# Kernel optimization log

Hardware: AMD Instinct MI355X
Metric: run time of the kernel (lower is better)

Reference implementation:

```python
import jax, jax.numpy as jnp
import numpy as np

D = 256        # model_dim
E = 4          # num_experts
H = 8          # attention heads
L = 8          # layers
P = 4          # patch size
IMG = 128
B = 8
NUM_CLASSES = 10
T = (IMG // P) ** 2  # 1024 tokens


def _ln(x, g, b):
    mu = jnp.mean(x, -1, keepdims=True)
    var = jnp.mean((x - mu) ** 2, -1, keepdims=True)
    return (x - mu) * jax.lax.rsqrt(var + 1e-5) * g + b


def setup_inputs() -> dict:
    key = jax.random.key(0)
    ks = jax.random.split(key, 24)
    n = lambda k, s, sc=0.02: jax.random.normal(k, s, jnp.float32) * sc
    return {
        "x": jax.random.normal(ks[0], (B, 3, IMG, IMG), jnp.float32),
        "patch_w": n(ks[1], (D, 3, P, P), 0.1),
        "patch_b": n(ks[2], (D,), 0.01),
        "pos_emb": n(ks[3], (1, T, D), 0.02),
        "router_w": n(ks[4], (E, D), 0.05),
        "router_b": n(ks[5], (E,), 0.01),
        "ln1_g": jnp.ones((L, D), jnp.float32),
        "ln1_b": jnp.zeros((L, D), jnp.float32),
        "q_w": n(ks[6], (L, D, D), 0.05),
        "q_b": n(ks[7], (L, D), 0.01),
        "k_w": n(ks[8], (L, D, D), 0.05),
        "k_b": n(ks[9], (L, D), 0.01),
        "v_w": n(ks[10], (L, D, D), 0.05),
        "v_b": n(ks[11], (L, D), 0.01),
        "o_w": n(ks[12], (L, D, D), 0.05),
        "o_b": n(ks[13], (L, D), 0.01),
        "ln2_g": jnp.ones((L, D), jnp.float32),
        "ln2_b": jnp.zeros((L, D), jnp.float32),
        "l1_w": n(ks[14], (L, 4 * D, D), 0.05),
        "l1_b": n(ks[15], (L, 4 * D), 0.01),
        "l2_w": n(ks[16], (L, D, 4 * D), 0.05),
        "l2_b": n(ks[17], (L, D), 0.01),
        "head_w": n(ks[18], (NUM_CLASSES, D), 0.05),
        "head_b": n(ks[19], (NUM_CLASSES,), 0.01),
        "alpha": jnp.full((1,), 0.5, jnp.float32),
    }


def reference(x, patch_w, patch_b, pos_emb, router_w, router_b, ln1_g, ln1_b,
              q_w, q_b, k_w, k_b, v_w, v_b, o_w, o_b, ln2_g, ln2_b,
              l1_w, l1_b, l2_w, l2_b, head_w, head_b, alpha):
    b = x.shape[0]
    # patch embed: Conv2d(3, D, P, stride=P)
    h = jax.lax.conv_general_dilated(x, patch_w, (P, P), 'VALID',
                                     dimension_numbers=('NCHW', 'OIHW', 'NCHW'))
    h = h + patch_b[None, :, None, None]
    tok = h.reshape(b, D, -1).transpose(0, 2, 1) + pos_emb   # [B,T,D]
    t = tok.shape[1]
    n_per = t // E  # uniform capacity: floor(T * 1/E)
    raw_prob = jax.nn.softmax(tok @ router_w.T + router_b, axis=-1)  # [B,T,E]
    # greedy routing: expert e takes top n_per of remaining tokens, rows zeroed after
    prob = raw_prob
    bidx = jnp.arange(b)[:, None]
    blocks, pblocks = [], []
    for e in range(E):
        _, idx = jax.lax.top_k(prob[:, :, e], n_per)            # [B,n_per]
        blocks.append(jnp.take_along_axis(tok, idx[:, :, None], axis=1))
        pblocks.append(jnp.take_along_axis(raw_prob, idx[:, :, None], axis=1))
        sel = jnp.zeros((b, t), prob.dtype).at[bidx, idx].set(1.0)
        prob = prob * (1.0 - sel)[:, :, None]
    xs = jnp.concatenate(blocks, axis=1)    # [B,T,D] expert-sorted
    rp = jnp.concatenate(pblocks, axis=1)   # [B,T,E]

    widths = [D // 2 ** e for e in range(E)]  # [256,128,64,32]
    scale = D ** -0.5                         # note: model_dim, not head_dim
    dh = D // H
    for l in range(L):
        # ---- nested-expert MHSA ----
        xn = _ln(xs, ln1_g[l], ln1_b[l])
        qs, ks_, vs = [], [], []
        for e in range(E):
            m = widths[e]
            blk = xn[:, e * n_per:(e + 1) * n_per, :m]
            qs.append(blk @ q_w[l][:, :m].T + q_b[l])
            ks_.append(blk @ k_w[l][:, :m].T + k_b[l])
            vs.append(blk @ v_w[l][:, :m].T + v_b[l])
        q = jnp.concatenate(qs, 1).reshape(b, t, H, dh).transpose(0, 2, 1, 3)
        k = jnp.concatenate(ks_, 1).reshape(b, t, H, dh).transpose(0, 2, 1, 3)
        v = jnp.concatenate(vs, 1).reshape(b, t, H, dh).transpose(0, 2, 1, 3)
        attn = jax.nn.softmax(jnp.einsum('bhqd,bhkd->bhqk', q, k) * scale, axis=-1)
        ao = jnp.einsum('bhqk,bhkd->bhqd', attn, v).transpose(0, 2, 1, 3).reshape(b, t, D)
        outs = []
        for e in range(E):
            m = widths[e]
            sl = slice(e * n_per, (e + 1) * n_per)
            o = ao[:, sl, :m] @ o_w[l][:m, :m].T + o_b[l][:m]
            o = jnp.pad(o, ((0, 0), (0, 0), (0, D - m)))
            outs.append(o + xs[:, sl, :])
        xs = jnp.concatenate(outs, 1)
        # ---- nested-expert MLP ----
        xn = _ln(xs, ln2_g[l], ln2_b[l])
        outs = []
        for e in range(E):
            m = widths[e]
            sl = slice(e * n_per, (e + 1) * n_per)
            blk = xn[:, sl, :m]
            inner = jax.nn.gelu(blk @ l1_w[l][:, :m].T + l1_b[l], approximate=False)
            outer = inner @ l2_w[l][:m, :].T + l2_b[l][:m]
            outer = jnp.pad(outer, ((0, 0), (0, 0), (0, D - m)))
            sf = (alpha[0] * rp[:, sl, e] + 1.0)[:, :, None]
            outs.append(xs[:, sl, :] + sf * outer)
        xs = jnp.concatenate(outs, 1)
    # classification head: mean pool + linear
    return jnp.mean(xs, axis=1) @ head_w.T + head_b
```

## Files before the change

### kernel.cpp

```cpp
#include <hip/hip_runtime.h>
#include <math.h>

#define D 256
#define E 4
#define H 8
#define LYR 8
#define IMG 128
#define BB 8
#define NC 10
#define T 1024
#define NPER 256
#define DH 32
#define D4 1024

using bf16x8 = __attribute__((ext_vector_type(8))) __bf16;
using bf16x4 = __attribute__((ext_vector_type(4))) __bf16;
using f32x4  = __attribute__((ext_vector_type(4))) float;

#define MFMA16(a, b, c) __builtin_amdgcn_mfma_f32_16x16x32_bf16((a), (b), (c), 0, 0, 0)

__device__ __forceinline__ void gload16(const void* g, void* l) {
    __builtin_amdgcn_global_load_lds(
        (const __attribute__((address_space(1))) void*)g,
        (__attribute__((address_space(3))) void*)l, 16, 0, 0);
}

__global__ void cast6(const float* __restrict__ s0, const float* __restrict__ s1,
                      const float* __restrict__ s2, const float* __restrict__ s3,
                      const float* __restrict__ s4, const float* __restrict__ s5,
                      __bf16* __restrict__ d0, __bf16* __restrict__ d1,
                      __bf16* __restrict__ d2, __bf16* __restrict__ d3,
                      __bf16* __restrict__ d4, __bf16* __restrict__ d5) {
    const long A4 = (long)LYR * D * D / 4;
    const long W4 = (long)LYR * D4 * D / 4;
    long i = (long)blockIdx.x * 256 + threadIdx.x;
    const float* s; __bf16* d; long off;
    if (i < 4 * A4) {
        int w = (int)(i / A4); off = i - (long)w * A4;
        s = w == 0 ? s0 : w == 1 ? s1 : w == 2 ? s2 : s3;
        d = w == 0 ? d0 : w == 1 ? d1 : w == 2 ? d2 : d3;
    } else {
        long j = i - 4 * A4;
        int w = (int)(j / W4); off = j - (long)w * W4;
        s = w ? s5 : s4; d = w ? d5 : d4;
    }
    float4 v = ((const float4*)s)[off];
    bf16x4 o;
    o[0] = (__bf16)v.x; o[1] = (__bf16)v.y; o[2] = (__bf16)v.z; o[3] = (__bf16)v.w;
    ((bf16x4*)d)[off] = o;
}

__global__ void patch_router(const float* __restrict__ x, const float* __restrict__ pw,
                             const float* __restrict__ pb, const float* __restrict__ pos,
                             const float* __restrict__ rw, const float* __restrict__ rb,
                             float* __restrict__ tok, float* __restrict__ rawp) {
    int t = blockIdx.x, b = blockIdx.y, d = threadIdx.x;
    __shared__ float sx[48];
    __shared__ float srow[D];
    __shared__ float slog[4];
    int ph = t >> 5, pwc = t & 31;
    if (d < 48) {
        int c = d >> 4, ij = d & 15, i = ij >> 2, j = ij & 3;
        sx[d] = x[(((long)b * 3 + c) * IMG + (ph * 4 + i)) * IMG + (pwc * 4 + j)];
    }
    __syncthreads();
    float acc = pb[d];
    #pragma unroll
    for (int kk = 0; kk < 48; ++kk) acc += sx[kk] * pw[d * 48 + kk];
    float val = acc + pos[(long)t * D + d];
    tok[((long)b * T + t) * D + d] = val;
    srow[d] = val;
    __syncthreads();
    int wv = d >> 6, lane = d & 63;
    float a = 0.f;
    for (int c = lane; c < D; c += 64) a += srow[c] * rw[wv * D + c];
    for (int off = 32; off; off >>= 1) a += __shfl_down(a, off);
    if (lane == 0) slog[wv] = a + rb[wv];
    __syncthreads();
    if (d == 0) {
        float l0 = slog[0], l1 = slog[1], l2 = slog[2], l3 = slog[3];
        float mx = fmaxf(fmaxf(l0, l1), fmaxf(l2, l3));
        float e0 = __expf(l0 - mx), e1 = __expf(l1 - mx), e2 = __expf(l2 - mx), e3 = __expf(l3 - mx);
        float inv = 1.0f / (e0 + e1 + e2 + e3);
        long row = (long)b * T + t;
        rawp[row * 4 + 0] = e0 * inv;
        rawp[row * 4 + 1] = e1 * inv;
        rawp[row * 4 + 2] = e2 * inv;
        rawp[row * 4 + 3] = e3 * inv;
    }
}

__global__ __launch_bounds__(1024) void route_topk(const float* __restrict__ rawp,
                                                   int* __restrict__ perm,
                                                   float* __restrict__ rpsel) {
    int b = blockIdx.x, tid = threadIdx.x;
    int lane = tid & 63, wv = tid >> 6;
    __shared__ unsigned hist[256];
    __shared__ unsigned long long ball[16];
    __shared__ int sb_bin, sb_rem;
    bool assigned = false;
    for (int e = 0; e < E; ++e) {
        float v = rawp[((long)b * T + tid) * E + e];
        unsigned key = assigned ? 0u : __float_as_uint(v);
        unsigned prefix = 0;
        int rem = NPER;
        #pragma unroll
        for (int pass = 3; pass >= 0; --pass) {
            int shift = pass * 8;
            if (tid < 256) hist[tid] = 0;
            __syncthreads();
            bool active = (pass == 3) || ((key >> (shift + 8)) == prefix);
            if (active) atomicAdd(&hist[(key >> shift) & 255], 1u);
            __syncthreads();
            if (tid < 64) {
                unsigned c[4], psum = 0;
                #pragma unroll
                for (int u = 0; u < 4; ++u) { c[u] = hist[tid * 4 + u]; psum += c[u]; }
                unsigned suf = psum;
                #pragma unroll
                for (int off = 1; off < 64; off <<= 1) {
                    unsigned o = __shfl_down(suf, off);
                    if (tid + off < 64) suf += o;
                }
                unsigned El = suf - psum;
                if (El < (unsigned)rem && (unsigned)rem <= suf) {
                    unsigned cab = El;
                    #pragma unroll
                    for (int u = 3; u >= 0; --u) {
                        if ((unsigned)rem > cab && (unsigned)rem <= cab + c[u]) {
                            sb_bin = tid * 4 + u;
                            sb_rem = (int)((unsigned)rem - cab);
                        }
                        cab += c[u];
                    }
                }
            }
            __syncthreads();
            prefix = (prefix << 8) | (unsigned)sb_bin;
            rem = sb_rem;
        }
        unsigned t = prefix;
        bool is_tie = (!assigned) && (key == t);
        unsigned long long mbt = __ballot(is_tie);
        if (lane == 0) ball[wv] = mbt;
        __syncthreads();
        int tierank = 0;
        for (int w2 = 0; w2 < wv; ++w2) tierank += __popcll(ball[w2]);
        tierank += __popcll(mbt & ((1ULL << lane) - 1));
        bool sel = (!assigned) && ((key > t) || (is_tie && tierank < rem));
        __syncthreads();
        unsigned long long mbs = __ballot(sel);
        if (lane == 0) ball[wv] = mbs;
        __syncthreads();
        int rank = 0;
        for (int w2 = 0; w2 < wv; ++w2) rank += __popcll(ball[w2]);
        rank += __popcll(mbs & ((1ULL << lane) - 1));
        if (sel) {
            perm[(long)b * T + e * NPER + rank] = tid;
            rpsel[(long)b * T + e * NPER + rank] = v;
            assigned = true;
        }
        __syncthreads();
    }
}

__global__ void gather_tokens(const float* __restrict__ tok, const int* __restrict__ perm,
                              float* __restrict__ xs) {
    int slot = blockIdx.x, b = blockIdx.y, d = threadIdx.x;
    int src = perm[(long)b * T + slot];
    xs[((long)b * T + slot) * D + d] = tok[((long)b * T + src) * D + d];
}

__device__ __forceinline__ void ln_rows32(const float* __restrict__ src,
                                          const float* __restrict__ g,
                                          const float* __restrict__ bta,
                                          __bf16 (*slds)[264], int tid) {
    int sub = tid & 15, rowh = tid >> 4;
    int col0 = sub * 16;
    float gv[16], bv[16];
    #pragma unroll
    for (int u = 0; u < 4; ++u) {
        float4 gg = *(const float4*)&g[col0 + 4 * u];
        float4 bb = *(const float4*)&bta[col0 + 4 * u];
        gv[4*u] = gg.x; gv[4*u+1] = gg.y; gv[4*u+2] = gg.z; gv[4*u+3] = gg.w;
        bv[4*u] = bb.x; bv[4*u+1] = bb.y; bv[4*u+2] = bb.z; bv[4*u+3] = bb.w;
    }
    #pragma unroll
    for (int half = 0; half < 2; ++half) {
        int r = rowh + half * 16;
        const float* rp = src + (long)r * D + col0;
        float v[16];
        #pragma unroll
        for (int u = 0; u < 4; ++u) {
            float4 vv = *(const float4*)&rp[4 * u];
            v[4*u] = vv.x; v[4*u+1] = vv.y; v[4*u+2] = vv.z; v[4*u+3] = vv.w;
        }
        float s = 0.f;
        #pragma unroll
        for (int u = 0; u < 16; ++u) s += v[u];
        #pragma unroll
        for (int mk = 1; mk < 16; mk <<= 1) s += __shfl_xor(s, mk);
        float mu = s * (1.0f / D);
        float s2 = 0.f;
        #pragma unroll
        for (int u = 0; u < 16; ++u) { v[u] -= mu; s2 += v[u] * v[u]; }
        #pragma unroll
        for (int mk = 1; mk < 16; mk <<= 1) s2 += __shfl_xor(s2, mk);
        float rstd = rsqrtf(s2 * (1.0f / D) + 1e-5f);
        bf16x8 o0, o1;
        #pragma unroll
        for (int u = 0; u < 8; ++u) o0[u] = (__bf16)(v[u] * rstd * gv[u] + bv[u]);
        #pragma unroll
        for (int u = 0; u < 8; ++u) o1[u] = (__bf16)(v[8+u] * rstd * gv[8+u] + bv[8+u]);
        *(bf16x8*)&slds[r][col0]     = o0;
        *(bf16x8*)&slds[r][col0 + 8] = o1;
    }
}

template<int RG, int K>
__device__ __forceinline__ void gemm_tile(
    const __bf16* __restrict__ A, int lda,
    const __bf16* __restrict__ W, int ldb,
    int lane, f32x4 (&acc)[RG][4])
{
    int lr = lane & 15, lk = (lane >> 4) * 8;
    const __bf16* a0 = A + (long)lr * lda + lk;
    const __bf16* b0 = W + (long)lr * ldb + lk;
    const __bf16* b1 = b0 + 16 * ldb;
    const __bf16* b2 = b0 + 32 * ldb;
    const __bf16* b3 = b0 + 48 * ldb;
    constexpr int CH = (K <= 256) ? K : 128;
    for (int kb = 0; kb < K; kb += CH) {
        #pragma unroll
        for (int ku = 0; ku < CH; ku += 32) {
            int k = kb + ku;
            bf16x8 av[RG];
            #pragma unroll
            for (int i = 0; i < RG; ++i) av[i] = *(const bf16x8*)(a0 + i * 16 * lda + k);
            bf16x8 bv0 = *(const bf16x8*)(b0 + k);
            bf16x8 bv1 = *(const bf16x8*)(b1 + k);
            bf16x8 bv2 = *(const bf16x8*)(b2 + k);
            bf16x8 bv3 = *(const bf16x8*)(b3 + k);
            #pragma unroll
            for (int i = 0; i < RG; ++i) {
                acc[i][0] = MFMA16(av[i], bv0, acc[i][0]);
                acc[i][1] = MFMA16(av[i], bv1, acc[i][1]);
                acc[i][2] = MFMA16(av[i], bv2, acc[i][2]);
                acc[i][3] = MFMA16(av[i], bv3, acc[i][3]);
            }
        }
    }
}

#define GEMM_K_DISPATCH(RG, Aexpr, lda, Wexpr, ldb, accv)                        \
    switch (m) {                                                                 \
      case 256: gemm_tile<RG, 256>(Aexpr, lda, Wexpr, ldb, lane, accv); break;   \
      case 128: gemm_tile<RG, 128>(Aexpr, lda, Wexpr, ldb, lane, accv); break;   \
      case 64:  gemm_tile<RG, 64>(Aexpr, lda, Wexpr, ldb, lane, accv); break;    \
      default:  gemm_tile<RG, 32>(Aexpr, lda, Wexpr, ldb, lane, accv); break;    \
    }

__global__ __launch_bounds__(256) void qkv_ln_gemm(
    const float* __restrict__ xs,
    const __bf16* __restrict__ qwb, const __bf16* __restrict__ kwb, const __bf16* __restrict__ vwb,
    const float* __restrict__ qb, const float* __restrict__ kb, const float* __restrict__ vb,
    const float* __restrict__ g, const float* __restrict__ bta,
    __bf16* __restrict__ Qb, __bf16* __restrict__ Kb, __bf16* __restrict__ Vt)
{
    int tid = threadIdx.x, lane = tid & 63, wid = tid >> 6;
    int tile = blockIdx.x, which = blockIdx.y, b = blockIdx.z;
    int row0 = tile * 32;
    int m = D >> (row0 >> 8);
    __shared__ __bf16 slds[32][264];
    ln_rows32(xs + ((long)b * T + row0) * D, g, bta, slds, tid);
    __syncthreads();
    const __bf16* W = which == 0 ? qwb : which == 1 ? kwb : vwb;
    const float* bias = which == 0 ? qb : which == 1 ? kb : vb;
    int ncol0 = wid * 64;
    const f32x4 vz = {0.f, 0.f, 0.f, 0.f};
    f32x4 acc[2][4];
    #pragma unroll
    for (int i = 0; i < 2; ++i) { acc[i][0]=vz; acc[i][1]=vz; acc[i][2]=vz; acc[i][3]=vz; }
    GEMM_K_DISPATCH(2, &slds[0][0], 264, W + (long)ncol0 * D, D, acc)
    int lr = lane & 15, rg = (lane >> 4) * 4;
    #pragma unroll
    for (int i = 0; i < 2; ++i) {
        int row = row0 + i * 16 + rg;
        #pragma unroll
        for (int j = 0; j < 4; ++j) {
            int n = ncol0 + j * 16 + lr;
            float bvs = bias[n];
            if (which == 2) {
                bf16x4 pk;
                #pragma unroll
                for (int r = 0; r < 4; ++r) pk[r] = (__bf16)(acc[i][j][r] + bvs);
                *(bf16x4*)&Vt[((long)b * D + n) * T + row] = pk;
            } else if (which == 0) {
                #pragma unroll
                for (int r = 0; r < 4; ++r)
                    Qb[((long)b * T + row + r) * D + n] = (__bf16)((acc[i][j][r] + bvs) * 0.0625f);
            } else {
                #pragma unroll
                for (int r = 0; r < 4; ++r)
                    Kb[((long)b * T + row + r) * D + n] = (__bf16)(acc[i][j][r] + bvs);
            }
        }
    }
}

__global__ __launch_bounds__(256) void attn_mfma(
    const __bf16* __restrict__ Qb, const __bf16* __restrict__ Kb,
    const __bf16* __restrict__ Vt, __bf16* __restrict__ aob)
{
    int bid = blockIdx.x;
    int bh = (bid & 7) * 8 + ((bid >> 3) & 7);
    int qt = bid >> 6;
    int b = bh >> 3, h = bh & 7;
    int tid = threadIdx.x;
    int lane = tid & 63, wave = tid >> 6;
    int lr = lane & 15, g = lane >> 4;
    int q0 = qt * 128 + wave * 32;
    __shared__ __bf16 plds[4][32][72];
    __shared__ __bf16 sK[2][4 * 64 * 8];
    __shared__ __bf16 sV[2][4 * 64 * 8];
    const f32x4 vz = {0.f, 0.f, 0.f, 0.f};
    bf16x8 qf[2];
    qf[0] = *(const bf16x8*)&Qb[((long)b * T + q0 + lr) * D + h * DH + g * 8];
    qf[1] = *(const bf16x8*)&Qb[((long)b * T + q0 + 16 + lr) * D + h * DH + g * 8];
    f32x4 acc[2][2] = {{vz, vz}, {vz, vz}};
    float ls[2] = {0.f, 0.f};
    const __bf16* kseg = Kb + ((long)b * T + 16 * wave + lr) * D + h * DH + g * 8;
    const __bf16* vseg = Vt + ((long)b * D + h * DH + (wave >> 1) * 16 + lr) * T
                            + 32 * (wave & 1) + 8 * g;

#define STAGE(BSEL, KC)                                   \
    {                                                     \
        gload16(kseg + (long)(KC) * D, &sK[BSEL][wave * 512]); \
        gload16(vseg + (KC),           &sV[BSEL][wave * 512]); \
    }

#define COMPUTE(BSEL)                                                                     \
    {                                                                                     \
        bf16x8 kf[4], vf[2][2];                                                           \
        _Pragma("unroll")                                                                 \
        for (int j = 0; j < 4; ++j)                                                       \
            kf[j] = *(const bf16x8*)&sK[BSEL][(j * 64 + lane) * 8];                       \
        _Pragma("unroll")                                                                 \
        for (int w2 = 0; w2 < 2; ++w2)                                                    \
            _Pragma("unroll")                                                             \
            for (int df = 0; df < 2; ++df)                                                \
                vf[w2][df] = *(const bf16x8*)&sV[BSEL][((df * 2 + w2) * 64 + lane) * 8];  \
        _Pragma("unroll")                                                                 \
        for (int qi = 0; qi < 2; ++qi) {                                                  \
            _Pragma("unroll")                                                             \
            for (int j = 0; j < 4; ++j) {                                                 \
                f32x4 s = MFMA16(kf[j], qf[qi], vz);                                      \
                float p0 = __expf(s[0]), p1 = __expf(s[1]);                               \
                float p2 = __expf(s[2]), p3 = __expf(s[3]);                               \
                ls[qi] += (p0 + p1) + (p2 + p3);                                          \
                bf16x4 pk;                                                                \
                pk[0] = (__bf16)p0; pk[1] = (__bf16)p1;                                   \
                pk[2] = (__bf16)p2; pk[3] = (__bf16)p3;                                   \
                *(bf16x4*)&plds[wave][qi * 16 + lr][16 * j + 4 * g] = pk;                 \
            }                                                                             \
        }                                                                                 \
        _Pragma("unroll")                                                                 \
        for (int qi = 0; qi < 2; ++qi) {                                                  \
            _Pragma("unroll")                                                             \
            for (int w2 = 0; w2 < 2; ++w2) {                                              \
                bf16x8 pa = *(const bf16x8*)&plds[wave][qi * 16 + lr][32 * w2 + 8 * g];   \
                acc[qi][0] = MFMA16(pa, vf[w2][0], acc[qi][0]);                           \
                acc[qi][1] = MFMA16(pa, vf[w2][1], acc[qi][1]);                           \
            }                                                                             \
        }                                                                                 \
    }

    STAGE(0, 0)
    __syncthreads();
    int bsel = 0;
    for (int kc = 0; kc < T; kc += 64) {
        if (kc + 64 < T) STAGE(bsel ^ 1, kc + 64)
        COMPUTE(bsel)
        __syncthreads();
        bsel ^= 1;
    }
#undef STAGE
#undef COMPUTE

    #pragma unroll
    for (int qi = 0; qi < 2; ++qi) {
        ls[qi] += __shfl_xor(ls[qi], 16);
        ls[qi] += __shfl_xor(ls[qi], 32);
        float inv = 1.0f / ls[qi];
        #pragma unroll
        for (int r = 0; r < 4; ++r) {
            float invr = __shfl(inv, 4 * g + r);
            long obase = ((long)b * T + q0 + qi * 16 + 4 * g + r) * D + h * DH;
            aob[obase + lr]      = (__bf16)(acc[qi][0][r] * invr);
            aob[obase + 16 + lr] = (__bf16)(acc[qi][1][r] * invr);
        }
    }
}

#define GEMM_PROLOGUE \
    int lane = threadIdx.x & 63, wid = threadIdx.x >> 6; \
    int wm = wid >> 1, wn = wid & 1; \
    int b = blockIdx.z >> 2, e = blockIdx.z & 3; \
    int m = D >> e; \
    const f32x4 vz = {0.f, 0.f, 0.f, 0.f}; \
    f32x4 acc[2][4]; \
    _Pragma("unroll") \
    for (int i = 0; i < 2; ++i) { acc[i][0]=vz; acc[i][1]=vz; acc[i][2]=vz; acc[i][3]=vz; }

__global__ __launch_bounds__(256) void oproj_gemm(
    const __bf16* __restrict__ aob, const __bf16* __restrict__ owb,
    const float* __restrict__ ob, float* __restrict__ xs)
{
    GEMM_PROLOGUE
    if ((int)blockIdx.y * 128 >= m) return;
    int ncol0 = blockIdx.y * 128 + wn * 64;
    int row0 = e * NPER + blockIdx.x * 64 + wm * 32;
    GEMM_K_DISPATCH(2, aob + ((long)b * T + row0) * D, D, owb + (long)ncol0 * D, D, acc)
    int lr = lane & 15, rg = (lane >> 4) * 4;
    #pragma unroll
    for (int i = 0; i < 2; ++i) {
        int row = row0 + i * 16 + rg;
        #pragma unroll
        for (int j = 0; j < 4; ++j) {
            int n = ncol0 + j * 16 + lr;
            if (n < m) {
                float bv = ob[n];
                #pragma unroll
                for (int r = 0; r < 4; ++r)
                    xs[((long)b * T + row + r) * D + n] += acc[i][j][r] + bv;
            }
        }
    }
}

__global__ __launch_bounds__(256) void mlp1_ln_gemm(
    const float* __restrict__ xs, const __bf16* __restrict__ w1b,
    const float* __restrict__ b1, const float* __restrict__ g, const float* __restrict__ bta,
    __bf16* __restrict__ innerb)
{
    int tid = threadIdx.x, lane = tid & 63, wid = tid >> 6;
    int tile = blockIdx.x, fq = blockIdx.y, b = blockIdx.z;
    int row0 = tile * 32;
    int m = D >> (row0 >> 8);
    __shared__ __bf16 slds[32][264];
    ln_rows32(xs + ((long)b * T + row0) * D, g, bta, slds, tid);
    __syncthreads();
    int ncol0 = fq * 256 + wid * 64;
    const f32x4 vz = {0.f, 0.f, 0.f, 0.f};
    f32x4 acc[2][4];
    #pragma unroll
    for (int i = 0; i < 2; ++i) { acc[i][0]=vz; acc[i][1]=vz; acc[i][2]=vz; acc[i][3]=vz; }
    GEMM_K_DISPATCH(2, &slds[0][0], 264, w1b + (long)ncol0 * D, D, acc)
    int lr = lane & 15, rg = (lane >> 4) * 4;
    #pragma unroll
    for (int i = 0; i < 2; ++i) {
        int row = row0 + i * 16 + rg;
        #pragma unroll
        for (int j = 0; j < 4; ++j) {
            int f = ncol0 + j * 16 + lr;
            float bv = b1[f];
            #pragma unroll
            for (int r = 0; r < 4; ++r) {
                float xv = acc[i][j][r] + bv;
                float gl = 0.5f * xv * (1.0f + erff(xv * 0.70710678118654752f));
                innerb[((long)b * T + row + r) * D4 + f] = (__bf16)gl;
            }
        }
    }
}

__global__ __launch_bounds__(256) void mlp2_gemm(
    const __bf16* __restrict__ innerb, const __bf16* __restrict__ w2b,
    const float* __restrict__ b2, const float* __restrict__ rpsel,
    const float* __restrict__ alpha, float* __restrict__ xs)
{
    GEMM_PROLOGUE
    if ((int)blockIdx.y * 128 >= m) return;
    int ncol0 = blockIdx.y * 128 + wn * 64;
    int row0 = e * NPER + blockIdx.x * 64 + wm * 32;
    gemm_tile<2, 1024>(innerb + ((long)b * T + row0) * D4, D4,
                       w2b + (long)ncol0 * D4, D4, lane, acc);
    int lr = lane & 15, rg = (lane >> 4) * 4;
    float a0 = alpha[0];
    #pragma unroll
    for (int i = 0; i < 2; ++i) {
        int row = row0 + i * 16 + rg;
        float sf[4];
        #pragma unroll
        for (int r = 0; r < 4; ++r) sf[r] = a0 * rpsel[(long)b * T + row + r] + 1.0f;
        #pragma unroll
        for (int j = 0; j < 4; ++j) {
            int n = ncol0 + j * 16 + lr;
            if (n < m) {
                float bv = b2[n];
                #pragma unroll
                for (int r = 0; r < 4; ++r)
                    xs[((long)b * T + row + r) * D + n] += sf[r] * (acc[i][j][r] + bv);
            }
        }
    }
}

__global__ void head_partial(const float* __restrict__ xs, float* __restrict__ part) {
    int c = blockIdx.x, b = blockIdx.y, d = threadIdx.x;
    const float* p = xs + ((long)b * T + c * 128) * D + d;
    float s = 0.f;
    #pragma unroll 8
    for (int i = 0; i < 128; ++i) s += p[(long)i * D];
    part[((long)b * 8 + c) * D + d] = s;
}

__global__ void head_final(const float* __restrict__ part, const float* __restrict__ hw,
                           const float* __restrict__ hb, float* __restrict__ out) {
    int b = blockIdx.x, d = threadIdx.x;
    __shared__ float smean[D];
    float s = 0.f;
    #pragma unroll
    for (int c = 0; c < 8; ++c) s += part[((long)b * 8 + c) * D + d];
    smean[d] = s * (1.0f / T);
    __syncthreads();
    if (d < NC) {
        float acc = hb[d];
        for (int c = 0; c < D; ++c) acc += smean[c] * hw[d * D + c];
        out[b * NC + d] = acc;
    }
}

extern "C" void kernel_launch(void* const* d_in, const int* in_sizes, int n_in,
                              void* d_out, int out_size, void* d_ws, size_t ws_size,
                              hipStream_t stream) {
    const float* x      = (const float*)d_in[0];
    const float* patchw = (const float*)d_in[1];
    const float* patchb = (const float*)d_in[2];
    const float* pos    = (const float*)d_in[3];
    const float* rw     = (const float*)d_in[4];
    const float* rb     = (const float*)d_in[5];
    const float* ln1g   = (const float*)d_in[6];
    const float* ln1b   = (const float*)d_in[7];
    const float* qw     = (const float*)d_in[8];
    const float* qbi    = (const float*)d_in[9];
    const float* kw     = (const float*)d_in[10];
    const float* kbi    = (const float*)d_in[11];
    const float* vw     = (const float*)d_in[12];
    const float* vbi    = (const float*)d_in[13];
    const float* ow     = (const float*)d_in[14];
    const float* obi    = (const float*)d_in[15];
    const float* ln2g   = (const float*)d_in[16];
    const float* ln2b   = (const float*)d_in[17];
    const float* l1w    = (const float*)d_in[18];
    const float* l1b    = (const float*)d_in[19];
    const float* l2w    = (const float*)d_in[20];
    const float* l2b    = (const float*)d_in[21];
    const float* hw     = (const float*)d_in[22];
    const float* hb     = (const float*)d_in[23];
    const float* alpha  = (const float*)d_in[24];

    char* p = (char*)d_ws;
    auto alloc = [&](size_t bytes) { void* r = (void*)p; p += (bytes + 255) & ~(size_t)255; return r; };
    const long NTD = (long)BB * T * D;

    float*  tok    = (float*)alloc(NTD * 4);
    float*  xs     = (float*)alloc(NTD * 4);
    float*  rawp   = (float*)alloc((long)BB * T * E * 4);
    float*  rpsel  = (float*)alloc((long)BB * T * 4);
    int*    perm   = (int*)alloc((long)BB * T * 4);
    float*  part   = (float*)alloc((long)BB * 8 * D * 4);
    __bf16* Qb     = (__bf16*)alloc(NTD * 2);
    __bf16* Kb     = (__bf16*)alloc(NTD * 2);
    __bf16* Vt     = (__bf16*)alloc(NTD * 2);
    __bf16* aob    = (__bf16*)alloc(NTD * 2);
    __bf16* innerb = (__bf16*)alloc((long)BB * T * D4 * 2);
    __bf16* qwb    = (__bf16*)alloc((long)LYR * D * D * 2);
    __bf16* kwb    = (__bf16*)alloc((long)LYR * D * D * 2);
    __bf16* vwb    = (__bf16*)alloc((long)LYR * D * D * 2);
    __bf16* owb    = (__bf16*)alloc((long)LYR * D * D * 2);
    __bf16* w1b    = (__bf16*)alloc((long)LYR * D4 * D * 2);
    __bf16* w2b    = (__bf16*)alloc((long)LYR * D * D4 * 2);

    cast6<<<6144, 256, 0, stream>>>(qw, kw, vw, ow, l1w, l2w, qwb, kwb, vwb, owb, w1b, w2b);

    patch_router<<<dim3(T, BB), 256, 0, stream>>>(x, patchw, patchb, pos, rw, rb, tok, rawp);
    route_topk<<<BB, 1024, 0, stream>>>(rawp, perm, rpsel);
    gather_tokens<<<dim3(T, BB), 256, 0, stream>>>(tok, perm, xs);

    for (int l = 0; l < LYR; ++l) {
        qkv_ln_gemm<<<dim3(32, 3, BB), 256, 0, stream>>>(
            xs, qwb + (long)l * D * D, kwb + (long)l * D * D, vwb + (long)l * D * D,
            qbi + l * D, kbi + l * D, vbi + l * D,
            ln1g + l * D, ln1b + l * D, Qb, Kb, Vt);
        attn_mfma<<<dim3(512), 256, 0, stream>>>(Qb, Kb, Vt, aob);
        oproj_gemm<<<dim3(4, 2, BB * E), 256, 0, stream>>>(
            aob, owb + (long)l * D * D, obi + l * D, xs);
        mlp1_ln_gemm<<<dim3(32, 4, BB), 256, 0, stream>>>(
            xs, w1b + (long)l * D4 * D, l1b + (long)l * D4,
            ln2g + l * D, ln2b + l * D, innerb);
        mlp2_gemm<<<dim3(4, 2, BB * E), 256, 0, stream>>>(
            innerb, w2b + (long)l * D * D4, l2b + l * D, rpsel, alpha, xs);
    }

    head_partial<<<dim3(8, BB), 256, 0, stream>>>(xs, part);
    head_final<<<BB, D, 0, stream>>>(part, hw, hb, (float*)d_out);
}
```

Baseline: 954.3 us.

## Compact expert tiles per wave and halve attention block size for occupancy

```diff
diff --git a/kernel.cpp b/kernel.cpp
--- a/kernel.cpp
+++ b/kernel.cpp
@@ -260,6 +260,13 @@
       default:  gemm_tile<RG, 32>(Aexpr, lda, Wexpr, ldb, lane, accv); break;    \
     }
 
+__device__ __forceinline__ void tile_map(int tau, int& e, int& rt, int& ct) {
+    if (tau < 64)       { e = 0; rt = tau >> 2; ct = tau & 3; }
+    else if (tau < 96)  { e = 1; int t2 = tau - 64; rt = t2 >> 1; ct = t2 & 1; }
+    else if (tau < 112) { e = 2; rt = tau - 96;  ct = 0; }
+    else                { e = 3; rt = tau - 112; ct = 0; }
+}
+
 __global__ __launch_bounds__(256) void qkv_ln_gemm(
     const float* __restrict__ xs,
     const __bf16* __restrict__ qwb, const __bf16* __restrict__ kwb, const __bf16* __restrict__ vwb,
@@ -308,7 +315,7 @@
     }
 }
 
-__global__ __launch_bounds__(256) void attn_mfma(
+__global__ __launch_bounds__(128) void attn_mfma(
     const __bf16* __restrict__ Qb, const __bf16* __restrict__ Kb,
     const __bf16* __restrict__ Vt, __bf16* __restrict__ aob)
 {
@@ -319,8 +326,8 @@
     int tid = threadIdx.x;
     int lane = tid & 63, wave = tid >> 6;
     int lr = lane & 15, g = lane >> 4;
-    int q0 = qt * 128 + wave * 32;
-    __shared__ __bf16 plds[4][32][72];
+    int q0 = qt * 64 + wave * 32;
+    __shared__ __bf16 plds[2][32][72];
     __shared__ __bf16 sK[2][4 * 64 * 8];
     __shared__ __bf16 sV[2][4 * 64 * 8];
     const f32x4 vz = {0.f, 0.f, 0.f, 0.f};
@@ -329,14 +336,20 @@
     qf[1] = *(const bf16x8*)&Qb[((long)b * T + q0 + 16 + lr) * D + h * DH + g * 8];
     f32x4 acc[2][2] = {{vz, vz}, {vz, vz}};
     float ls[2] = {0.f, 0.f};
-    const __bf16* kseg = Kb + ((long)b * T + 16 * wave + lr) * D + h * DH + g * 8;
-    const __bf16* vseg = Vt + ((long)b * D + h * DH + (wave >> 1) * 16 + lr) * T
-                            + 32 * (wave & 1) + 8 * g;
-
-#define STAGE(BSEL, KC)                                   \
-    {                                                     \
-        gload16(kseg + (long)(KC) * D, &sK[BSEL][wave * 512]); \
-        gload16(vseg + (KC),           &sV[BSEL][wave * 512]); \
+    int j0 = 2 * wave, j1 = 2 * wave + 1;
+    const __bf16* kseg0 = Kb + ((long)b * T + 16 * j0 + lr) * D + h * DH + g * 8;
+    const __bf16* kseg1 = Kb + ((long)b * T + 16 * j1 + lr) * D + h * DH + g * 8;
+    const __bf16* vseg0 = Vt + ((long)b * D + h * DH + (j0 >> 1) * 16 + lr) * T
+                             + 32 * (j0 & 1) + 8 * g;
+    const __bf16* vseg1 = Vt + ((long)b * D + h * DH + (j1 >> 1) * 16 + lr) * T
+                             + 32 * (j1 & 1) + 8 * g;
+
+#define STAGE(BSEL, KC)                                        \
+    {                                                          \
+        gload16(kseg0 + (long)(KC) * D, &sK[BSEL][j0 * 512]);  \
+        gload16(kseg1 + (long)(KC) * D, &sK[BSEL][j1 * 512]);  \
+        gload16(vseg0 + (KC),           &sV[BSEL][j0 * 512]);  \
+        gload16(vseg1 + (KC),           &sV[BSEL][j1 * 512]);  \
     }
 
 #define COMPUTE(BSEL)                                                                     \
@@ -402,38 +415,31 @@
     }
 }
 
-#define GEMM_PROLOGUE \
-    int lane = threadIdx.x & 63, wid = threadIdx.x >> 6; \
-    int wm = wid >> 1, wn = wid & 1; \
-    int b = blockIdx.z >> 2, e = blockIdx.z & 3; \
-    int m = D >> e; \
-    const f32x4 vz = {0.f, 0.f, 0.f, 0.f}; \
-    f32x4 acc[2][4]; \
-    _Pragma("unroll") \
-    for (int i = 0; i < 2; ++i) { acc[i][0]=vz; acc[i][1]=vz; acc[i][2]=vz; acc[i][3]=vz; }
-
 __global__ __launch_bounds__(256) void oproj_gemm(
     const __bf16* __restrict__ aob, const __bf16* __restrict__ owb,
     const float* __restrict__ ob, float* __restrict__ xs)
 {
-    GEMM_PROLOGUE
-    if ((int)blockIdx.y * 128 >= m) return;
-    int ncol0 = blockIdx.y * 128 + wn * 64;
-    int row0 = e * NPER + blockIdx.x * 64 + wm * 32;
-    GEMM_K_DISPATCH(2, aob + ((long)b * T + row0) * D, D, owb + (long)ncol0 * D, D, acc)
+    int tid = threadIdx.x, lane = tid & 63, wid = tid >> 6;
+    int gw = blockIdx.x * 4 + wid;
+    int b = gw >> 7, tau = gw & 127;
+    int e, rt, ct;
+    tile_map(tau, e, rt, ct);
+    int m = D >> e;
+    int row0 = e * NPER + rt * 16;
+    int ncol0 = ct * 64;
+    const f32x4 vz = {0.f, 0.f, 0.f, 0.f};
+    f32x4 acc[1][4] = {{vz, vz, vz, vz}};
+    GEMM_K_DISPATCH(1, aob + ((long)b * T + row0) * D, D, owb + (long)ncol0 * D, D, acc)
     int lr = lane & 15, rg = (lane >> 4) * 4;
-    #pragma unroll
-    for (int i = 0; i < 2; ++i) {
-        int row = row0 + i * 16 + rg;
-        #pragma unroll
-        for (int j = 0; j < 4; ++j) {
-            int n = ncol0 + j * 16 + lr;
-            if (n < m) {
-                float bv = ob[n];
-                #pragma unroll
-                for (int r = 0; r < 4; ++r)
-                    xs[((long)b * T + row + r) * D + n] += acc[i][j][r] + bv;
-            }
+    int row = row0 + rg;
+    #pragma unroll
+    for (int j = 0; j < 4; ++j) {
+        int n = ncol0 + j * 16 + lr;
+        if (n < m) {
+            float bv = ob[n];
+            #pragma unroll
+            for (int r = 0; r < 4; ++r)
+                xs[((long)b * T + row + r) * D + n] += acc[0][j][r] + bv;
         }
     }
 }
@@ -479,29 +485,32 @@
     const float* __restrict__ b2, const float* __restrict__ rpsel,
     const float* __restrict__ alpha, float* __restrict__ xs)
 {
-    GEMM_PROLOGUE
-    if ((int)blockIdx.y * 128 >= m) return;
-    int ncol0 = blockIdx.y * 128 + wn * 64;
-    int row0 = e * NPER + blockIdx.x * 64 + wm * 32;
-    gemm_tile<2, 1024>(innerb + ((long)b * T + row0) * D4, D4,
+    int tid = threadIdx.x, lane = tid & 63, wid = tid >> 6;
+    int gw = blockIdx.x * 4 + wid;
+    int b = gw >> 7, tau = gw & 127;
+    int e, rt, ct;
+    tile_map(tau, e, rt, ct);
+    int m = D >> e;
+    int row0 = e * NPER + rt * 16;
+    int ncol0 = ct * 64;
+    const f32x4 vz = {0.f, 0.f, 0.f, 0.f};
+    f32x4 acc[1][4] = {{vz, vz, vz, vz}};
+    gemm_tile<1, 1024>(innerb + ((long)b * T + row0) * D4, D4,
                        w2b + (long)ncol0 * D4, D4, lane, acc);
     int lr = lane & 15, rg = (lane >> 4) * 4;
+    int row = row0 + rg;
     float a0 = alpha[0];
-    #pragma unroll
-    for (int i = 0; i < 2; ++i) {
-        int row = row0 + i * 16 + rg;
-        float sf[4];
-        #pragma unroll
-        for (int r = 0; r < 4; ++r) sf[r] = a0 * rpsel[(long)b * T + row + r] + 1.0f;
-        #pragma unroll
-        for (int j = 0; j < 4; ++j) {
-            int n = ncol0 + j * 16 + lr;
-            if (n < m) {
-                float bv = b2[n];
-                #pragma unroll
-                for (int r = 0; r < 4; ++r)
-                    xs[((long)b * T + row + r) * D + n] += sf[r] * (acc[i][j][r] + bv);
-            }
+    float sf[4];
+    #pragma unroll
+    for (int r = 0; r < 4; ++r) sf[r] = a0 * rpsel[(long)b * T + row + r] + 1.0f;
+    #pragma unroll
+    for (int j = 0; j < 4; ++j) {
+        int n = ncol0 + j * 16 + lr;
+        if (n < m) {
+            float bv = b2[n];
+            #pragma unroll
+            for (int r = 0; r < 4; ++r)
+                xs[((long)b * T + row + r) * D + n] += sf[r] * (acc[0][j][r] + bv);
         }
     }
 }
@@ -593,13 +602,13 @@
             xs, qwb + (long)l * D * D, kwb + (long)l * D * D, vwb + (long)l * D * D,
             qbi + l * D, kbi + l * D, vbi + l * D,
             ln1g + l * D, ln1b + l * D, Qb, Kb, Vt);
-        attn_mfma<<<dim3(512), 256, 0, stream>>>(Qb, Kb, Vt, aob);
-        oproj_gemm<<<dim3(4, 2, BB * E), 256, 0, stream>>>(
+        attn_mfma<<<dim3(1024), 128, 0, stream>>>(Qb, Kb, Vt, aob);
+        oproj_gemm<<<dim3(256), 256, 0, stream>>>(
             aob, owb + (long)l * D * D, obi + l * D, xs);
         mlp1_ln_gemm<<<dim3(32, 4, BB), 256, 0, stream>>>(
             xs, w1b + (long)l * D4 * D, l1b + (long)l * D4,
             ln2g + l * D, ln2b + l * D, innerb);
-        mlp2_gemm<<<dim3(4, 2, BB * E), 256, 0, stream>>>(
+        mlp2_gemm<<<dim3(256), 256, 0, stream>>>(
             innerb, w2b + (long)l * D * D4, l2b + l * D, rpsel, alpha, xs);
     }
 
```

Measured after the change: 905.8 us. -5.1%, faster.
